# Kernel optimization log

Measured on AMD Instinct MI355X. Metric: run time of the kernel, lower is better.

Reference implementation:

```python
import jax, jax.numpy as jnp
import numpy as np

N_NODES = 500000
N_EDGES = 5000000
IN_CH, OUT_CH = 16, 8


def setup_inputs() -> dict:
    key = jax.random.key(0)
    k1, k2, k3, k4, k5 = jax.random.split(key, 5)
    x = jax.random.normal(k1, (N_NODES, IN_CH), dtype=jnp.float32)
    src = jax.random.randint(k2, (N_EDGES,), 0, N_NODES, dtype=jnp.int64)
    dst = jax.random.randint(k3, (N_EDGES,), 0, N_NODES, dtype=jnp.int64)
    edge_index = jnp.stack([src, dst], axis=0)
    # PyG Linear: weight [out, in], Glorot init; GCNConv bias init zeros
    bound = np.sqrt(6.0 / (IN_CH + OUT_CH))
    W = jax.random.uniform(k4, (OUT_CH, IN_CH), dtype=jnp.float32, minval=-bound, maxval=bound)
    b = jnp.zeros((OUT_CH,), dtype=jnp.float32)
    return {"x": x, "edge_index": edge_index, "W": W, "b": b}


def reference(x, edge_index, W, b):
    """GCNConv(16, 8) with defaults: add_self_loops=True, normalize=True, bias.
    out = D^{-1/2} (A + I) D^{-1/2} X W^T + b, scatter by target index."""
    N = x.shape[0]
    loops = jnp.arange(N, dtype=edge_index.dtype)
    src = jnp.concatenate([edge_index[0], loops])  # [E + N]
    dst = jnp.concatenate([edge_index[1], loops])
    # degree of self-loop-augmented graph, accumulated at target nodes
    deg = jax.ops.segment_sum(jnp.ones(src.shape[0], dtype=x.dtype), dst, num_segments=N)
    dinv = jnp.where(deg > 0, jax.lax.rsqrt(deg), jnp.zeros_like(deg))
    norm = dinv[src] * dinv[dst]  # [E + N]
    h = x @ W.T  # [N, OUT_CH]
    msgs = norm[:, None] * h[src]  # gather + scale, [E + N, OUT_CH]
    out = jax.ops.segment_sum(msgs, dst, num_segments=N) + b
    return out
```

## Files before the change

### kernel.cpp

```cpp
#include <hip/hip_runtime.h>
#include <hip/hip_fp16.h>

#define IN_CH 16
#define OUT_CH 8

#define NT 256
#define EPT 24
#define TILE (NT*EPT)
#define NBUK 512
#define BSHIFT 10
#define BNODES 1024
#define BMASK 1023
#define SRCBITS 19
#define SRCMASK 0x7FFFF
#define CAP 11264
#define RPT 44

typedef float __attribute__((ext_vector_type(4))) fv4;

__global__ void __launch_bounds__(NT) k_bin(const int4* __restrict__ src4,
                                            const int4* __restrict__ dst4, int E,
                                            int* __restrict__ gcur,
                                            unsigned* __restrict__ gbuf) {
    __shared__ int hist[NBUK];
    __shared__ int lofs[NBUK];
    __shared__ int gofs[NBUK];
    __shared__ int wsum[4];
    __shared__ unsigned stage[TILE];
    __shared__ unsigned short posb[TILE];

    int t = threadIdx.x;
    long base = (long)blockIdx.x * TILE;
    int cnt = E - (int)base;
    if (cnt > TILE) cnt = TILE;

    for (int j = t; j < NBUK; j += NT) hist[j] = 0;
    __syncthreads();

    unsigned v[EPT];
    int bk[EPT];
    int rk[EPT];
#pragma unroll
    for (int k = 0; k < EPT / 4; k++) {
        int i4 = t + k * NT;
        if (4 * i4 < cnt) {
            int4 s = src4[base / 4 + i4];
            int4 d = dst4[base / 4 + i4];
            int ss[4] = {s.x, s.y, s.z, s.w};
            int dd[4] = {d.x, d.y, d.z, d.w};
#pragma unroll
            for (int j = 0; j < 4; j++) {
                int q = 4 * k + j;
                bk[q] = dd[j] >> BSHIFT;
                v[q] = ((unsigned)(dd[j] & BMASK) << SRCBITS) | (unsigned)ss[j];
                rk[q] = atomicAdd(&hist[bk[q]], 1);
            }
        } else {
#pragma unroll
            for (int j = 0; j < 4; j++) bk[4 * k + j] = -1;
        }
    }
    __syncthreads();

    int a0 = hist[2 * t], a1 = hist[2 * t + 1];
    int ts = a0 + a1;
    int lane = t & 63, wv = t >> 6;
    int inc = ts;
#pragma unroll
    for (int d = 1; d < 64; d <<= 1) {
        int y = __shfl_up(inc, d);
        if (lane >= d) inc += y;
    }
    if (lane == 63) wsum[wv] = inc;
    __syncthreads();
    int wpre = 0;
#pragma unroll
    for (int w = 0; w < 4; w++) wpre += (w < wv) ? wsum[w] : 0;
    int excl = wpre + inc - ts;

    lofs[2 * t] = excl;
    lofs[2 * t + 1] = excl + a0;
    if (a0 > 0) gofs[2 * t] = atomicAdd(&gcur[2 * t], a0) - excl;
    if (a1 > 0) gofs[2 * t + 1] = atomicAdd(&gcur[2 * t + 1], a1) - (excl + a0);
    __syncthreads();

#pragma unroll
    for (int k = 0; k < EPT; k++) {
        if (bk[k] >= 0) {
            int slot = lofs[bk[k]] + rk[k];
            stage[slot] = v[k];
            posb[slot] = (unsigned short)bk[k];
        }
    }
    __syncthreads();

#pragma unroll
    for (int k = 0; k < EPT; k++) {
        int idx = t + k * NT;
        if (idx < cnt) {
            int b2 = posb[idx];
            gbuf[(size_t)b2 * CAP + idx + gofs[b2]] = stage[idx];
        }
    }
}

__global__ void __launch_bounds__(NT) k_degtrans(const unsigned* __restrict__ gbuf,
                                                 const int* __restrict__ gcur,
                                                 const float* __restrict__ x,
                                                 const float* __restrict__ W,
                                                 uint4* __restrict__ hp16, int N) {
    __shared__ int hist[BNODES];
    __shared__ float Ws[OUT_CH * IN_CH];

    int b = blockIdx.x, t = threadIdx.x;
    int cnt = gcur[b];
    const unsigned* p = gbuf + (size_t)b * CAP;

    if (t < OUT_CH * IN_CH) Ws[t] = W[t];
    for (int j = t; j < BNODES; j += NT) hist[j] = 0;
    __syncthreads();

    int n4 = (cnt + 3) >> 2;
    for (int i4 = t; i4 < n4; i4 += NT) {
        uint4 vv = *(const uint4*)(p + 4 * i4);
        unsigned vs[4] = {vv.x, vv.y, vv.z, vv.w};
#pragma unroll
        for (int j = 0; j < 4; j++)
            if (4 * i4 + j < cnt) atomicAdd(&hist[vs[j] >> SRCBITS], 1);
    }
    __syncthreads();

    int n0 = (b << BSHIFT) + 4 * t;
#pragma unroll
    for (int k = 0; k < 4; k++) {
        int n = n0 + k;
        if (n >= N) break;
        float di = rsqrtf(1.0f + (float)hist[4 * t + k]);
        const float4* xp = (const float4*)(x + (size_t)n * IN_CH);
        float4 a0 = xp[0], a1 = xp[1], a2 = xp[2], a3 = xp[3];
        float xi[IN_CH] = {a0.x, a0.y, a0.z, a0.w, a1.x, a1.y, a1.z, a1.w,
                           a2.x, a2.y, a2.z, a2.w, a3.x, a3.y, a3.z, a3.w};
        float h[OUT_CH];
#pragma unroll
        for (int o = 0; o < OUT_CH; o++) {
            float s = 0.0f;
#pragma unroll
            for (int i = 0; i < IN_CH; i++) s += xi[i] * Ws[o * IN_CH + i];
            h[o] = s * di;
        }
        union { uint4 u; __half2 h2[4]; } pk;
        pk.h2[0] = __float22half2_rn(make_float2(h[0], h[1]));
        pk.h2[1] = __float22half2_rn(make_float2(h[2], h[3]));
        pk.h2[2] = __float22half2_rn(make_float2(h[4], h[5]));
        pk.h2[3] = __float22half2_rn(make_float2(h[6], h[7]));
        hp16[n] = pk.u;
    }
}

__device__ __forceinline__ void acc_add(float* a, uint4 g) {
    union { uint4 u; __half2 h2[4]; } pk;
    pk.u = g;
    float2 f0 = __half22float2(pk.h2[0]);
    float2 f1 = __half22float2(pk.h2[1]);
    float2 f2 = __half22float2(pk.h2[2]);
    float2 f3 = __half22float2(pk.h2[3]);
    a[0] += f0.x; a[1] += f0.y; a[2] += f1.x; a[3] += f1.y;
    a[4] += f2.x; a[5] += f2.y; a[6] += f3.x; a[7] += f3.y;
}

__global__ void __launch_bounds__(NT) k_sortgather(const unsigned* __restrict__ gbuf,
                                                   const int* __restrict__ gcur,
                                                   const uint4* __restrict__ hp16,
                                                   const float* __restrict__ bias,
                                                   float* __restrict__ out, int N) {
    __shared__ unsigned sorted[CAP];
    __shared__ int hist[BNODES];
    __shared__ int wsum[4];

    int b = blockIdx.x, t = threadIdx.x;
    int cnt = gcur[b];
    const unsigned* p = gbuf + (size_t)b * CAP;

    for (int j = t; j < BNODES; j += NT) hist[j] = 0;
    __syncthreads();

    unsigned v[RPT];
    int rk[RPT];
#pragma unroll
    for (int k4 = 0; k4 < RPT / 4; k4++) {
        int idx = 4 * t + k4 * 4 * NT;
        uint4 vv = *(const uint4*)(p + idx);
        unsigned vs[4] = {vv.x, vv.y, vv.z, vv.w};
#pragma unroll
        for (int j = 0; j < 4; j++) {
            int k = 4 * k4 + j;
            if (idx + j < cnt) {
                v[k] = vs[j];
                rk[k] = atomicAdd(&hist[v[k] >> SRCBITS], 1);
            }
        }
    }
    __syncthreads();

    int h0 = hist[4 * t], h1 = hist[4 * t + 1], h2 = hist[4 * t + 2], h3 = hist[4 * t + 3];
    int ts = h0 + h1 + h2 + h3;
    int lane = t & 63, wv = t >> 6;
    int inc = ts;
#pragma unroll
    for (int d = 1; d < 64; d <<= 1) {
        int y = __shfl_up(inc, d);
        if (lane >= d) inc += y;
    }
    if (lane == 63) wsum[wv] = inc;
    __syncthreads();
    int wpre = 0;
#pragma unroll
    for (int w = 0; w < 4; w++) wpre += (w < wv) ? wsum[w] : 0;
    int e0 = wpre + inc - ts;
    int e1 = e0 + h0, e2 = e1 + h1, e3 = e2 + h2;
    hist[4 * t] = e0; hist[4 * t + 1] = e1; hist[4 * t + 2] = e2; hist[4 * t + 3] = e3;
    __syncthreads();

#pragma unroll
    for (int k4 = 0; k4 < RPT / 4; k4++) {
#pragma unroll
        for (int j = 0; j < 4; j++) {
            int k = 4 * k4 + j;
            int idx = 4 * t + k4 * 4 * NT + j;
            if (idx < cnt) {
                int slot = hist[v[k] >> SRCBITS] + rk[k];
                sorted[slot] = v[k] & SRCMASK;
            }
        }
    }
    __syncthreads();

    int n0 = (b << BSHIFT) + 4 * t;
    int eS[4] = {e0, e1, e2, e3};
    int hS[4] = {h0, h1, h2, h3};

    float bb[OUT_CH];
#pragma unroll
    for (int o = 0; o < OUT_CH; o++) bb[o] = bias[o];

#pragma unroll
    for (int k = 0; k < 4; k++) {
        int n = n0 + k;
        if (n >= N) break;

        float a[OUT_CH];
        acc_add((float*)a, hp16[n]);
#pragma unroll
        for (int o = 0; o < OUT_CH; o++) a[o] = a[o];
        {
            union { uint4 u; __half2 h2[4]; } pk;
            pk.u = hp16[n];
            float2 f0 = __half22float2(pk.h2[0]);
            float2 f1 = __half22float2(pk.h2[1]);
            float2 f2 = __half22float2(pk.h2[2]);
            float2 f3 = __half22float2(pk.h2[3]);
            a[0] = f0.x; a[1] = f0.y; a[2] = f1.x; a[3] = f1.y;
            a[4] = f2.x; a[5] = f2.y; a[6] = f3.x; a[7] = f3.y;
        }

        int e = eS[k], end = eS[k] + hS[k];
        for (; e + 3 < end; e += 4) {
            unsigned s0 = sorted[e], s1 = sorted[e + 1];
            unsigned s2 = sorted[e + 2], s3 = sorted[e + 3];
            uint4 g0 = hp16[s0];
            uint4 g1 = hp16[s1];
            uint4 g2 = hp16[s2];
            uint4 g3 = hp16[s3];
            acc_add(a, g0); acc_add(a, g1); acc_add(a, g2); acc_add(a, g3);
        }
        for (; e < end; e++) {
            uint4 g0 = hp16[sorted[e]];
            acc_add(a, g0);
        }

        float di = rsqrtf(1.0f + (float)hS[k]);
        fv4 o0, o1;
#pragma unroll
        for (int j = 0; j < 4; j++) {
            o0[j] = a[j] * di + bb[j];
            o1[j] = a[4 + j] * di + bb[4 + j];
        }
        __builtin_nontemporal_store(o0, (fv4*)(out + (size_t)n * OUT_CH));
        __builtin_nontemporal_store(o1, (fv4*)(out + (size_t)n * OUT_CH) + 1);
    }
}

extern "C" void kernel_launch(void* const* d_in, const int* in_sizes, int n_in,
                              void* d_out, int out_size, void* d_ws, size_t ws_size,
                              hipStream_t stream) {
    const float* x  = (const float*)d_in[0];
    const int*   ei = (const int*)d_in[1];
    const float* W  = (const float*)d_in[2];
    const float* b  = (const float*)d_in[3];
    float* out = (float*)d_out;

    const int N = in_sizes[0] / IN_CH;
    const int E = in_sizes[1] / 2;
    const int* src = ei;
    const int* dst = ei + E;

    const int nbuckets = (N + BNODES - 1) >> BSHIFT;

    int*      gcur = (int*)d_ws;
    uint4*    hp16 = (uint4*)(gcur + NBUK);
    unsigned* gbuf = (unsigned*)(hp16 + N);

    const int tiles = (E + TILE - 1) / TILE;

    (void)hipMemsetAsync(gcur, 0, NBUK * sizeof(int), stream);
    k_bin<<<tiles, NT, 0, stream>>>((const int4*)src, (const int4*)dst, E, gcur, gbuf);
    k_degtrans<<<nbuckets, NT, 0, stream>>>(gbuf, gcur, x, W, hp16, N);
    k_sortgather<<<nbuckets, NT, 0, stream>>>(gbuf, gcur, hp16, b, out, N);
}
```

Before: 215.0 us.

## Replace per-bucket counting sort with LDS atomic accumulation of gathered messages

The final kernel no longer counting-sorts each bucket's edges by destination before a per-node gather loop. Instead each thread gathers source features for eight edges at a time and accumulates them into a shared-memory per-channel accumulator with float atomics, also counting degree atomically. This removes the sort passes, scan and large register arrays, and exposes more independent gathers in flight. In exchange it issues nine LDS atomics per edge and makes the summation order nondeterministic.

```diff
diff --git a/kernel.cpp b/kernel.cpp
--- a/kernel.cpp
+++ b/kernel.cpp
@@ -14,9 +14,9 @@
 #define SRCBITS 19
 #define SRCMASK 0x7FFFF
 #define CAP 11264
-#define RPT 44
 
 typedef float __attribute__((ext_vector_type(4))) fv4;
+typedef unsigned __attribute__((ext_vector_type(4))) uv4;
 
 __global__ void __launch_bounds__(NT) k_bin(const int4* __restrict__ src4,
                                             const int4* __restrict__ dst4, int E,
@@ -157,136 +157,89 @@
     }
 }
 
-__device__ __forceinline__ void acc_add(float* a, uint4 g) {
-    union { uint4 u; __half2 h2[4]; } pk;
-    pk.u = g;
-    float2 f0 = __half22float2(pk.h2[0]);
-    float2 f1 = __half22float2(pk.h2[1]);
-    float2 f2 = __half22float2(pk.h2[2]);
-    float2 f3 = __half22float2(pk.h2[3]);
-    a[0] += f0.x; a[1] += f0.y; a[2] += f1.x; a[3] += f1.y;
-    a[4] += f2.x; a[5] += f2.y; a[6] += f3.x; a[7] += f3.y;
-}
-
-__global__ void __launch_bounds__(NT) k_sortgather(const unsigned* __restrict__ gbuf,
-                                                   const int* __restrict__ gcur,
-                                                   const uint4* __restrict__ hp16,
-                                                   const float* __restrict__ bias,
-                                                   float* __restrict__ out, int N) {
-    __shared__ unsigned sorted[CAP];
-    __shared__ int hist[BNODES];
-    __shared__ int wsum[4];
+__global__ void __launch_bounds__(NT) k_gatheracc(const unsigned* __restrict__ gbuf,
+                                                  const int* __restrict__ gcur,
+                                                  const uint4* __restrict__ hp16,
+                                                  const float* __restrict__ bias,
+                                                  float* __restrict__ out, int N) {
+    __shared__ float sacc[OUT_CH][BNODES];
+    __shared__ int shist[BNODES];
 
     int b = blockIdx.x, t = threadIdx.x;
     int cnt = gcur[b];
     const unsigned* p = gbuf + (size_t)b * CAP;
 
-    for (int j = t; j < BNODES; j += NT) hist[j] = 0;
-    __syncthreads();
-
-    unsigned v[RPT];
-    int rk[RPT];
-#pragma unroll
-    for (int k4 = 0; k4 < RPT / 4; k4++) {
-        int idx = 4 * t + k4 * 4 * NT;
-        uint4 vv = *(const uint4*)(p + idx);
-        unsigned vs[4] = {vv.x, vv.y, vv.z, vv.w};
-#pragma unroll
-        for (int j = 0; j < 4; j++) {
-            int k = 4 * k4 + j;
-            if (idx + j < cnt) {
-                v[k] = vs[j];
-                rk[k] = atomicAdd(&hist[v[k] >> SRCBITS], 1);
+    float4* sz = (float4*)&sacc[0][0];
+#pragma unroll
+    for (int j = 0; j < (OUT_CH * BNODES / 4) / NT; j++)
+        sz[t + j * NT] = make_float4(0.f, 0.f, 0.f, 0.f);
+    ((int4*)shist)[t] = make_int4(0, 0, 0, 0);
+    __syncthreads();
+
+    for (int base = 8 * t; base < cnt; base += 8 * NT) {
+        uv4 va = __builtin_nontemporal_load((const uv4*)(p + base));
+        uv4 vb = __builtin_nontemporal_load((const uv4*)(p + base) + 1);
+        unsigned vs[8] = {va.x, va.y, va.z, va.w, vb.x, vb.y, vb.z, vb.w};
+        int m = cnt - base;
+        uint4 g[8];
+        int ld[8];
+#pragma unroll
+        for (int j = 0; j < 8; j++) {
+            ld[j] = (int)(vs[j] >> SRCBITS);
+            if (j < m) g[j] = hp16[vs[j] & SRCMASK];
+        }
+#pragma unroll
+        for (int j = 0; j < 8; j++) {
+            if (j < m) {
+                union { uint4 u; __half2 h2[4]; } pk;
+                pk.u = g[j];
+                float2 f0 = __half22float2(pk.h2[0]);
+                float2 f1 = __half22float2(pk.h2[1]);
+                float2 f2 = __half22float2(pk.h2[2]);
+                float2 f3 = __half22float2(pk.h2[3]);
+                int d = ld[j];
+                atomicAdd(&shist[d], 1);
+                atomicAdd(&sacc[0][d], f0.x);
+                atomicAdd(&sacc[1][d], f0.y);
+                atomicAdd(&sacc[2][d], f1.x);
+                atomicAdd(&sacc[3][d], f1.y);
+                atomicAdd(&sacc[4][d], f2.x);
+                atomicAdd(&sacc[5][d], f2.y);
+                atomicAdd(&sacc[6][d], f3.x);
+                atomicAdd(&sacc[7][d], f3.y);
             }
         }
     }
     __syncthreads();
 
-    int h0 = hist[4 * t], h1 = hist[4 * t + 1], h2 = hist[4 * t + 2], h3 = hist[4 * t + 3];
-    int ts = h0 + h1 + h2 + h3;
-    int lane = t & 63, wv = t >> 6;
-    int inc = ts;
-#pragma unroll
-    for (int d = 1; d < 64; d <<= 1) {
-        int y = __shfl_up(inc, d);
-        if (lane >= d) inc += y;
-    }
-    if (lane == 63) wsum[wv] = inc;
-    __syncthreads();
-    int wpre = 0;
-#pragma unroll
-    for (int w = 0; w < 4; w++) wpre += (w < wv) ? wsum[w] : 0;
-    int e0 = wpre + inc - ts;
-    int e1 = e0 + h0, e2 = e1 + h1, e3 = e2 + h2;
-    hist[4 * t] = e0; hist[4 * t + 1] = e1; hist[4 * t + 2] = e2; hist[4 * t + 3] = e3;
-    __syncthreads();
-
-#pragma unroll
-    for (int k4 = 0; k4 < RPT / 4; k4++) {
-#pragma unroll
-        for (int j = 0; j < 4; j++) {
-            int k = 4 * k4 + j;
-            int idx = 4 * t + k4 * 4 * NT + j;
-            if (idx < cnt) {
-                int slot = hist[v[k] >> SRCBITS] + rk[k];
-                sorted[slot] = v[k] & SRCMASK;
-            }
-        }
-    }
-    __syncthreads();
-
-    int n0 = (b << BSHIFT) + 4 * t;
-    int eS[4] = {e0, e1, e2, e3};
-    int hS[4] = {h0, h1, h2, h3};
-
     float bb[OUT_CH];
 #pragma unroll
     for (int o = 0; o < OUT_CH; o++) bb[o] = bias[o];
 
 #pragma unroll
-    for (int k = 0; k < 4; k++) {
-        int n = n0 + k;
-        if (n >= N) break;
-
-        float a[OUT_CH];
-        acc_add((float*)a, hp16[n]);
-#pragma unroll
-        for (int o = 0; o < OUT_CH; o++) a[o] = a[o];
-        {
+    for (int k = 0; k < BNODES / NT; k++) {
+        int ln = t + k * NT;
+        int n = (b << BSHIFT) + ln;
+        if (n < N) {
             union { uint4 u; __half2 h2[4]; } pk;
             pk.u = hp16[n];
             float2 f0 = __half22float2(pk.h2[0]);
             float2 f1 = __half22float2(pk.h2[1]);
             float2 f2 = __half22float2(pk.h2[2]);
             float2 f3 = __half22float2(pk.h2[3]);
-            a[0] = f0.x; a[1] = f0.y; a[2] = f1.x; a[3] = f1.y;
-            a[4] = f2.x; a[5] = f2.y; a[6] = f3.x; a[7] = f3.y;
-        }
-
-        int e = eS[k], end = eS[k] + hS[k];
-        for (; e + 3 < end; e += 4) {
-            unsigned s0 = sorted[e], s1 = sorted[e + 1];
-            unsigned s2 = sorted[e + 2], s3 = sorted[e + 3];
-            uint4 g0 = hp16[s0];
-            uint4 g1 = hp16[s1];
-            uint4 g2 = hp16[s2];
-            uint4 g3 = hp16[s3];
-            acc_add(a, g0); acc_add(a, g1); acc_add(a, g2); acc_add(a, g3);
-        }
-        for (; e < end; e++) {
-            uint4 g0 = hp16[sorted[e]];
-            acc_add(a, g0);
-        }
-
-        float di = rsqrtf(1.0f + (float)hS[k]);
-        fv4 o0, o1;
-#pragma unroll
-        for (int j = 0; j < 4; j++) {
-            o0[j] = a[j] * di + bb[j];
-            o1[j] = a[4 + j] * di + bb[4 + j];
-        }
-        __builtin_nontemporal_store(o0, (fv4*)(out + (size_t)n * OUT_CH));
-        __builtin_nontemporal_store(o1, (fv4*)(out + (size_t)n * OUT_CH) + 1);
+            float di = rsqrtf(1.0f + (float)shist[ln]);
+            fv4 o0, o1;
+            o0[0] = (sacc[0][ln] + f0.x) * di + bb[0];
+            o0[1] = (sacc[1][ln] + f0.y) * di + bb[1];
+            o0[2] = (sacc[2][ln] + f1.x) * di + bb[2];
+            o0[3] = (sacc[3][ln] + f1.y) * di + bb[3];
+            o1[0] = (sacc[4][ln] + f2.x) * di + bb[4];
+            o1[1] = (sacc[5][ln] + f2.y) * di + bb[5];
+            o1[2] = (sacc[6][ln] + f3.x) * di + bb[6];
+            o1[3] = (sacc[7][ln] + f3.y) * di + bb[7];
+            __builtin_nontemporal_store(o0, (fv4*)(out + (size_t)n * OUT_CH));
+            __builtin_nontemporal_store(o1, (fv4*)(out + (size_t)n * OUT_CH) + 1);
+        }
     }
 }
 
@@ -315,5 +268,5 @@
     (void)hipMemsetAsync(gcur, 0, NBUK * sizeof(int), stream);
     k_bin<<<tiles, NT, 0, stream>>>((const int4*)src, (const int4*)dst, E, gcur, gbuf);
     k_degtrans<<<nbuckets, NT, 0, stream>>>(gbuf, gcur, x, W, hp16, N);
-    k_sortgather<<<nbuckets, NT, 0, stream>>>(gbuf, gcur, hp16, b, out, N);
-}
+    k_gatheracc<<<nbuckets, NT, 0, stream>>>(gbuf, gcur, hp16, b, out, N);
+}
```

Measured after the change: 378.8 us. +76.2%, slower.

## Move in-bucket sort into degree kernel and gather with one thread per node

Applied to the files above, without the earlier changes.

The per-bucket counting sort now runs in the degree/transform kernel, which writes the sorted source list back to global memory along with per-node row offsets (CSR). The gather kernel becomes a lightweight one-node-per-thread pass over 4x more blocks, with no LDS and no register-heavy staging. This is meant to raise occupancy and latency hiding in the random-gather phase. The cost is an extra global write and re-read of the sorted edges plus a row-offset array.

```diff
diff --git a/kernel.cpp b/kernel.cpp
--- a/kernel.cpp
+++ b/kernel.cpp
@@ -15,6 +15,7 @@
 #define SRCMASK 0x7FFFF
 #define CAP 11264
 #define RPT 44
+#define SPLITN 4
 
 typedef float __attribute__((ext_vector_type(4))) fv4;
 
@@ -104,83 +105,22 @@
     }
 }
 
-__global__ void __launch_bounds__(NT) k_degtrans(const unsigned* __restrict__ gbuf,
-                                                 const int* __restrict__ gcur,
-                                                 const float* __restrict__ x,
-                                                 const float* __restrict__ W,
-                                                 uint4* __restrict__ hp16, int N) {
+__global__ void __launch_bounds__(NT) k_degsort(unsigned* __restrict__ gbuf,
+                                                const int* __restrict__ gcur,
+                                                const float* __restrict__ x,
+                                                const float* __restrict__ W,
+                                                uint4* __restrict__ hp16,
+                                                int* __restrict__ rowofs, int N) {
+    __shared__ unsigned sorted[CAP];
     __shared__ int hist[BNODES];
     __shared__ float Ws[OUT_CH * IN_CH];
+    __shared__ int wsum[4];
 
     int b = blockIdx.x, t = threadIdx.x;
     int cnt = gcur[b];
-    const unsigned* p = gbuf + (size_t)b * CAP;
+    unsigned* p = gbuf + (size_t)b * CAP;
 
     if (t < OUT_CH * IN_CH) Ws[t] = W[t];
-    for (int j = t; j < BNODES; j += NT) hist[j] = 0;
-    __syncthreads();
-
-    int n4 = (cnt + 3) >> 2;
-    for (int i4 = t; i4 < n4; i4 += NT) {
-        uint4 vv = *(const uint4*)(p + 4 * i4);
-        unsigned vs[4] = {vv.x, vv.y, vv.z, vv.w};
-#pragma unroll
-        for (int j = 0; j < 4; j++)
-            if (4 * i4 + j < cnt) atomicAdd(&hist[vs[j] >> SRCBITS], 1);
-    }
-    __syncthreads();
-
-    int n0 = (b << BSHIFT) + 4 * t;
-#pragma unroll
-    for (int k = 0; k < 4; k++) {
-        int n = n0 + k;
-        if (n >= N) break;
-        float di = rsqrtf(1.0f + (float)hist[4 * t + k]);
-        const float4* xp = (const float4*)(x + (size_t)n * IN_CH);
-        float4 a0 = xp[0], a1 = xp[1], a2 = xp[2], a3 = xp[3];
-        float xi[IN_CH] = {a0.x, a0.y, a0.z, a0.w, a1.x, a1.y, a1.z, a1.w,
-                           a2.x, a2.y, a2.z, a2.w, a3.x, a3.y, a3.z, a3.w};
-        float h[OUT_CH];
-#pragma unroll
-        for (int o = 0; o < OUT_CH; o++) {
-            float s = 0.0f;
-#pragma unroll
-            for (int i = 0; i < IN_CH; i++) s += xi[i] * Ws[o * IN_CH + i];
-            h[o] = s * di;
-        }
-        union { uint4 u; __half2 h2[4]; } pk;
-        pk.h2[0] = __float22half2_rn(make_float2(h[0], h[1]));
-        pk.h2[1] = __float22half2_rn(make_float2(h[2], h[3]));
-        pk.h2[2] = __float22half2_rn(make_float2(h[4], h[5]));
-        pk.h2[3] = __float22half2_rn(make_float2(h[6], h[7]));
-        hp16[n] = pk.u;
-    }
-}
-
-__device__ __forceinline__ void acc_add(float* a, uint4 g) {
-    union { uint4 u; __half2 h2[4]; } pk;
-    pk.u = g;
-    float2 f0 = __half22float2(pk.h2[0]);
-    float2 f1 = __half22float2(pk.h2[1]);
-    float2 f2 = __half22float2(pk.h2[2]);
-    float2 f3 = __half22float2(pk.h2[3]);
-    a[0] += f0.x; a[1] += f0.y; a[2] += f1.x; a[3] += f1.y;
-    a[4] += f2.x; a[5] += f2.y; a[6] += f3.x; a[7] += f3.y;
-}
-
-__global__ void __launch_bounds__(NT) k_sortgather(const unsigned* __restrict__ gbuf,
-                                                   const int* __restrict__ gcur,
-                                                   const uint4* __restrict__ hp16,
-                                                   const float* __restrict__ bias,
-                                                   float* __restrict__ out, int N) {
-    __shared__ unsigned sorted[CAP];
-    __shared__ int hist[BNODES];
-    __shared__ int wsum[4];
-
-    int b = blockIdx.x, t = threadIdx.x;
-    int cnt = gcur[b];
-    const unsigned* p = gbuf + (size_t)b * CAP;
-
     for (int j = t; j < BNODES; j += NT) hist[j] = 0;
     __syncthreads();
 
@@ -218,6 +158,8 @@
     for (int w = 0; w < 4; w++) wpre += (w < wv) ? wsum[w] : 0;
     int e0 = wpre + inc - ts;
     int e1 = e0 + h0, e2 = e1 + h1, e3 = e2 + h2;
+    int4 eo = make_int4(e0, e1, e2, e3);
+    *(int4*)(rowofs + (b << BSHIFT) + 4 * t) = eo;
     hist[4 * t] = e0; hist[4 * t + 1] = e1; hist[4 * t + 2] = e2; hist[4 * t + 3] = e3;
     __syncthreads();
 
@@ -235,59 +177,106 @@
     }
     __syncthreads();
 
+    int n4 = (cnt + 3) >> 2;
+    for (int i4 = t; i4 < n4; i4 += NT)
+        ((uint4*)p)[i4] = ((const uint4*)sorted)[i4];
+
     int n0 = (b << BSHIFT) + 4 * t;
-    int eS[4] = {e0, e1, e2, e3};
-    int hS[4] = {h0, h1, h2, h3};
-
-    float bb[OUT_CH];
-#pragma unroll
-    for (int o = 0; o < OUT_CH; o++) bb[o] = bias[o];
-
+    int hh[4] = {h0, h1, h2, h3};
 #pragma unroll
     for (int k = 0; k < 4; k++) {
         int n = n0 + k;
         if (n >= N) break;
-
-        float a[OUT_CH];
-        acc_add((float*)a, hp16[n]);
-#pragma unroll
-        for (int o = 0; o < OUT_CH; o++) a[o] = a[o];
-        {
-            union { uint4 u; __half2 h2[4]; } pk;
-            pk.u = hp16[n];
+        float di = rsqrtf(1.0f + (float)hh[k]);
+        const float4* xp = (const float4*)(x + (size_t)n * IN_CH);
+        float4 a0 = xp[0], a1 = xp[1], a2 = xp[2], a3 = xp[3];
+        float xi[IN_CH] = {a0.x, a0.y, a0.z, a0.w, a1.x, a1.y, a1.z, a1.w,
+                           a2.x, a2.y, a2.z, a2.w, a3.x, a3.y, a3.z, a3.w};
+        float h[OUT_CH];
+#pragma unroll
+        for (int o = 0; o < OUT_CH; o++) {
+            float s = 0.0f;
+#pragma unroll
+            for (int i = 0; i < IN_CH; i++) s += xi[i] * Ws[o * IN_CH + i];
+            h[o] = s * di;
+        }
+        union { uint4 u; __half2 h2[4]; } pk;
+        pk.h2[0] = __float22half2_rn(make_float2(h[0], h[1]));
+        pk.h2[1] = __float22half2_rn(make_float2(h[2], h[3]));
+        pk.h2[2] = __float22half2_rn(make_float2(h[4], h[5]));
+        pk.h2[3] = __float22half2_rn(make_float2(h[6], h[7]));
+        hp16[n] = pk.u;
+    }
+}
+
+__global__ void __launch_bounds__(NT) k_gather(const unsigned* __restrict__ gbuf,
+                                               const int* __restrict__ gcur,
+                                               const int* __restrict__ rowofs,
+                                               const uint4* __restrict__ hp16,
+                                               const float* __restrict__ bias,
+                                               float* __restrict__ out, int N) {
+    int bx = blockIdx.x;
+    int b = bx / SPLITN, q = bx % SPLITN;
+    int t = threadIdx.x;
+    int ln = q * NT + t;
+    int n = (b << BSHIFT) + ln;
+    if (n >= N) return;
+
+    int s = rowofs[(b << BSHIFT) + ln];
+    int e = (ln == BNODES - 1) ? gcur[b] : rowofs[(b << BSHIFT) + ln + 1];
+    const unsigned* p = gbuf + (size_t)b * CAP;
+
+    float a[OUT_CH];
+    {
+        union { uint4 u; __half2 h2[4]; } pk;
+        pk.u = hp16[n];
+        float2 f0 = __half22float2(pk.h2[0]);
+        float2 f1 = __half22float2(pk.h2[1]);
+        float2 f2 = __half22float2(pk.h2[2]);
+        float2 f3 = __half22float2(pk.h2[3]);
+        a[0] = f0.x; a[1] = f0.y; a[2] = f1.x; a[3] = f1.y;
+        a[4] = f2.x; a[5] = f2.y; a[6] = f3.x; a[7] = f3.y;
+    }
+
+    int i = s;
+    for (; i + 3 < e; i += 4) {
+        unsigned s0 = p[i], s1 = p[i + 1], s2 = p[i + 2], s3 = p[i + 3];
+        uint4 g0 = hp16[s0];
+        uint4 g1 = hp16[s1];
+        uint4 g2 = hp16[s2];
+        uint4 g3 = hp16[s3];
+        union { uint4 u; __half2 h2[4]; } pk;
+#pragma unroll
+        for (int jj = 0; jj < 4; jj++) {
+            pk.u = (jj == 0) ? g0 : (jj == 1) ? g1 : (jj == 2) ? g2 : g3;
             float2 f0 = __half22float2(pk.h2[0]);
             float2 f1 = __half22float2(pk.h2[1]);
             float2 f2 = __half22float2(pk.h2[2]);
             float2 f3 = __half22float2(pk.h2[3]);
-            a[0] = f0.x; a[1] = f0.y; a[2] = f1.x; a[3] = f1.y;
-            a[4] = f2.x; a[5] = f2.y; a[6] = f3.x; a[7] = f3.y;
-        }
-
-        int e = eS[k], end = eS[k] + hS[k];
-        for (; e + 3 < end; e += 4) {
-            unsigned s0 = sorted[e], s1 = sorted[e + 1];
-            unsigned s2 = sorted[e + 2], s3 = sorted[e + 3];
-            uint4 g0 = hp16[s0];
-            uint4 g1 = hp16[s1];
-            uint4 g2 = hp16[s2];
-            uint4 g3 = hp16[s3];
-            acc_add(a, g0); acc_add(a, g1); acc_add(a, g2); acc_add(a, g3);
-        }
-        for (; e < end; e++) {
-            uint4 g0 = hp16[sorted[e]];
-            acc_add(a, g0);
-        }
-
-        float di = rsqrtf(1.0f + (float)hS[k]);
-        fv4 o0, o1;
-#pragma unroll
-        for (int j = 0; j < 4; j++) {
-            o0[j] = a[j] * di + bb[j];
-            o1[j] = a[4 + j] * di + bb[4 + j];
-        }
-        __builtin_nontemporal_store(o0, (fv4*)(out + (size_t)n * OUT_CH));
-        __builtin_nontemporal_store(o1, (fv4*)(out + (size_t)n * OUT_CH) + 1);
-    }
+            a[0] += f0.x; a[1] += f0.y; a[2] += f1.x; a[3] += f1.y;
+            a[4] += f2.x; a[5] += f2.y; a[6] += f3.x; a[7] += f3.y;
+        }
+    }
+    for (; i < e; i++) {
+        union { uint4 u; __half2 h2[4]; } pk;
+        pk.u = hp16[p[i]];
+        float2 f0 = __half22float2(pk.h2[0]);
+        float2 f1 = __half22float2(pk.h2[1]);
+        float2 f2 = __half22float2(pk.h2[2]);
+        float2 f3 = __half22float2(pk.h2[3]);
+        a[0] += f0.x; a[1] += f0.y; a[2] += f1.x; a[3] += f1.y;
+        a[4] += f2.x; a[5] += f2.y; a[6] += f3.x; a[7] += f3.y;
+    }
+
+    float di = rsqrtf(1.0f + (float)(e - s));
+    fv4 o0, o1;
+#pragma unroll
+    for (int j = 0; j < 4; j++) {
+        o0[j] = a[j] * di + bias[j];
+        o1[j] = a[4 + j] * di + bias[4 + j];
+    }
+    __builtin_nontemporal_store(o0, (fv4*)(out + (size_t)n * OUT_CH));
+    __builtin_nontemporal_store(o1, (fv4*)(out + (size_t)n * OUT_CH) + 1);
 }
 
 extern "C" void kernel_launch(void* const* d_in, const int* in_sizes, int n_in,
@@ -306,14 +295,15 @@
 
     const int nbuckets = (N + BNODES - 1) >> BSHIFT;
 
-    int*      gcur = (int*)d_ws;
-    uint4*    hp16 = (uint4*)(gcur + NBUK);
-    unsigned* gbuf = (unsigned*)(hp16 + N);
+    int*      gcur   = (int*)d_ws;
+    uint4*    hp16   = (uint4*)(gcur + NBUK);
+    unsigned* gbuf   = (unsigned*)(hp16 + N);
+    int*      rowofs = (int*)(gbuf + (size_t)NBUK * CAP);
 
     const int tiles = (E + TILE - 1) / TILE;
 
     (void)hipMemsetAsync(gcur, 0, NBUK * sizeof(int), stream);
     k_bin<<<tiles, NT, 0, stream>>>((const int4*)src, (const int4*)dst, E, gcur, gbuf);
-    k_degtrans<<<nbuckets, NT, 0, stream>>>(gbuf, gcur, x, W, hp16, N);
-    k_sortgather<<<nbuckets, NT, 0, stream>>>(gbuf, gcur, hp16, b, out, N);
+    k_degsort<<<nbuckets, NT, 0, stream>>>(gbuf, gcur, x, W, hp16, rowofs, N);
+    k_gather<<<nbuckets * SPLITN, NT, 0, stream>>>(gbuf, gcur, rowofs, hp16, b, out, N);
 }
```

Result: slower. 225.9 us (+5.1%).

## Compute degrees via global atomics in binning and split features into half-planes

Applied to the files above, without the earlier changes.

Degree counting moves into the binning kernel as global atomicAdds on a zeroed degree array, so the transform kernel becomes a flat per-node kernel that no longer re-reads the bucketed edge buffer. The sort/gather kernel now takes per-node counts from the degree array to build offsets directly and places edges with shared atomics. The fp16 features are split into two 8-byte planes gathered in two passes, which halves the bytes per random gather but doubles the number of gathers. The cost is 5M global atomics added to the binning kernel and an extra memset of the degree buffer.

```diff
diff --git a/kernel.cpp b/kernel.cpp
--- a/kernel.cpp
+++ b/kernel.cpp
@@ -14,14 +14,15 @@
 #define SRCBITS 19
 #define SRCMASK 0x7FFFF
 #define CAP 11264
-#define RPT 44
 
 typedef float __attribute__((ext_vector_type(4))) fv4;
+typedef unsigned __attribute__((ext_vector_type(4))) uv4;
 
 __global__ void __launch_bounds__(NT) k_bin(const int4* __restrict__ src4,
                                             const int4* __restrict__ dst4, int E,
                                             int* __restrict__ gcur,
-                                            unsigned* __restrict__ gbuf) {
+                                            unsigned* __restrict__ gbuf,
+                                            unsigned* __restrict__ deg) {
     __shared__ int hist[NBUK];
     __shared__ int lofs[NBUK];
     __shared__ int gofs[NBUK];
@@ -54,6 +55,7 @@
                 bk[q] = dd[j] >> BSHIFT;
                 v[q] = ((unsigned)(dd[j] & BMASK) << SRCBITS) | (unsigned)ss[j];
                 rk[q] = atomicAdd(&hist[bk[q]], 1);
+                atomicAdd(&deg[dd[j]], 1u);
             }
         } else {
 #pragma unroll
@@ -104,105 +106,62 @@
     }
 }
 
-__global__ void __launch_bounds__(NT) k_degtrans(const unsigned* __restrict__ gbuf,
-                                                 const int* __restrict__ gcur,
-                                                 const float* __restrict__ x,
-                                                 const float* __restrict__ W,
-                                                 uint4* __restrict__ hp16, int N) {
-    __shared__ int hist[BNODES];
+__global__ void __launch_bounds__(NT) k_trans(const float* __restrict__ x,
+                                              const float* __restrict__ W,
+                                              const unsigned* __restrict__ deg,
+                                              uint2* __restrict__ hpA,
+                                              uint2* __restrict__ hpB, int N) {
     __shared__ float Ws[OUT_CH * IN_CH];
+    int t = threadIdx.x;
+    if (t < OUT_CH * IN_CH) Ws[t] = W[t];
+    __syncthreads();
+    int n = blockIdx.x * NT + t;
+    if (n >= N) return;
+    float di = rsqrtf(1.0f + (float)deg[n]);
+    const fv4* xp = (const fv4*)(x + (size_t)n * IN_CH);
+    fv4 a0 = __builtin_nontemporal_load(xp);
+    fv4 a1 = __builtin_nontemporal_load(xp + 1);
+    fv4 a2 = __builtin_nontemporal_load(xp + 2);
+    fv4 a3 = __builtin_nontemporal_load(xp + 3);
+    float xi[IN_CH] = {a0[0], a0[1], a0[2], a0[3], a1[0], a1[1], a1[2], a1[3],
+                       a2[0], a2[1], a2[2], a2[3], a3[0], a3[1], a3[2], a3[3]};
+    float h[OUT_CH];
+#pragma unroll
+    for (int o = 0; o < OUT_CH; o++) {
+        float s = 0.0f;
+#pragma unroll
+        for (int i = 0; i < IN_CH; i++) s += xi[i] * Ws[o * IN_CH + i];
+        h[o] = s * di;
+    }
+    union { uint2 u; __half2 h2[2]; } pa, pb;
+    pa.h2[0] = __float22half2_rn(make_float2(h[0], h[1]));
+    pa.h2[1] = __float22half2_rn(make_float2(h[2], h[3]));
+    pb.h2[0] = __float22half2_rn(make_float2(h[4], h[5]));
+    pb.h2[1] = __float22half2_rn(make_float2(h[6], h[7]));
+    hpA[n] = pa.u;
+    hpB[n] = pb.u;
+}
+
+__global__ void __launch_bounds__(NT) k_sortgather(const unsigned* __restrict__ gbuf,
+                                                   const int* __restrict__ gcur,
+                                                   const unsigned* __restrict__ deg,
+                                                   const uint2* __restrict__ hpA,
+                                                   const uint2* __restrict__ hpB,
+                                                   const float* __restrict__ bias,
+                                                   float* __restrict__ out, int N) {
+    __shared__ unsigned sorted[CAP];
+    __shared__ int ofs[BNODES];
+    __shared__ int cnt1[BNODES];
+    __shared__ int wsum[4];
 
     int b = blockIdx.x, t = threadIdx.x;
     int cnt = gcur[b];
     const unsigned* p = gbuf + (size_t)b * CAP;
 
-    if (t < OUT_CH * IN_CH) Ws[t] = W[t];
-    for (int j = t; j < BNODES; j += NT) hist[j] = 0;
-    __syncthreads();
-
-    int n4 = (cnt + 3) >> 2;
-    for (int i4 = t; i4 < n4; i4 += NT) {
-        uint4 vv = *(const uint4*)(p + 4 * i4);
-        unsigned vs[4] = {vv.x, vv.y, vv.z, vv.w};
-#pragma unroll
-        for (int j = 0; j < 4; j++)
-            if (4 * i4 + j < cnt) atomicAdd(&hist[vs[j] >> SRCBITS], 1);
-    }
-    __syncthreads();
-
-    int n0 = (b << BSHIFT) + 4 * t;
-#pragma unroll
-    for (int k = 0; k < 4; k++) {
-        int n = n0 + k;
-        if (n >= N) break;
-        float di = rsqrtf(1.0f + (float)hist[4 * t + k]);
-        const float4* xp = (const float4*)(x + (size_t)n * IN_CH);
-        float4 a0 = xp[0], a1 = xp[1], a2 = xp[2], a3 = xp[3];
-        float xi[IN_CH] = {a0.x, a0.y, a0.z, a0.w, a1.x, a1.y, a1.z, a1.w,
-                           a2.x, a2.y, a2.z, a2.w, a3.x, a3.y, a3.z, a3.w};
-        float h[OUT_CH];
-#pragma unroll
-        for (int o = 0; o < OUT_CH; o++) {
-            float s = 0.0f;
-#pragma unroll
-            for (int i = 0; i < IN_CH; i++) s += xi[i] * Ws[o * IN_CH + i];
-            h[o] = s * di;
-        }
-        union { uint4 u; __half2 h2[4]; } pk;
-        pk.h2[0] = __float22half2_rn(make_float2(h[0], h[1]));
-        pk.h2[1] = __float22half2_rn(make_float2(h[2], h[3]));
-        pk.h2[2] = __float22half2_rn(make_float2(h[4], h[5]));
-        pk.h2[3] = __float22half2_rn(make_float2(h[6], h[7]));
-        hp16[n] = pk.u;
-    }
-}
-
-__device__ __forceinline__ void acc_add(float* a, uint4 g) {
-    union { uint4 u; __half2 h2[4]; } pk;
-    pk.u = g;
-    float2 f0 = __half22float2(pk.h2[0]);
-    float2 f1 = __half22float2(pk.h2[1]);
-    float2 f2 = __half22float2(pk.h2[2]);
-    float2 f3 = __half22float2(pk.h2[3]);
-    a[0] += f0.x; a[1] += f0.y; a[2] += f1.x; a[3] += f1.y;
-    a[4] += f2.x; a[5] += f2.y; a[6] += f3.x; a[7] += f3.y;
-}
-
-__global__ void __launch_bounds__(NT) k_sortgather(const unsigned* __restrict__ gbuf,
-                                                   const int* __restrict__ gcur,
-                                                   const uint4* __restrict__ hp16,
-                                                   const float* __restrict__ bias,
-                                                   float* __restrict__ out, int N) {
-    __shared__ unsigned sorted[CAP];
-    __shared__ int hist[BNODES];
-    __shared__ int wsum[4];
-
-    int b = blockIdx.x, t = threadIdx.x;
-    int cnt = gcur[b];
-    const unsigned* p = gbuf + (size_t)b * CAP;
-
-    for (int j = t; j < BNODES; j += NT) hist[j] = 0;
-    __syncthreads();
-
-    unsigned v[RPT];
-    int rk[RPT];
-#pragma unroll
-    for (int k4 = 0; k4 < RPT / 4; k4++) {
-        int idx = 4 * t + k4 * 4 * NT;
-        uint4 vv = *(const uint4*)(p + idx);
-        unsigned vs[4] = {vv.x, vv.y, vv.z, vv.w};
-#pragma unroll
-        for (int j = 0; j < 4; j++) {
-            int k = 4 * k4 + j;
-            if (idx + j < cnt) {
-                v[k] = vs[j];
-                rk[k] = atomicAdd(&hist[v[k] >> SRCBITS], 1);
-            }
-        }
-    }
-    __syncthreads();
-
-    int h0 = hist[4 * t], h1 = hist[4 * t + 1], h2 = hist[4 * t + 2], h3 = hist[4 * t + 3];
+    ((int4*)cnt1)[t] = make_int4(0, 0, 0, 0);
+
+    uint4 dg4 = *(const uint4*)(deg + (b << BSHIFT) + 4 * t);
+    int h0 = (int)dg4.x, h1 = (int)dg4.y, h2 = (int)dg4.z, h3 = (int)dg4.w;
     int ts = h0 + h1 + h2 + h3;
     int lane = t & 63, wv = t >> 6;
     int inc = ts;
@@ -218,18 +177,19 @@
     for (int w = 0; w < 4; w++) wpre += (w < wv) ? wsum[w] : 0;
     int e0 = wpre + inc - ts;
     int e1 = e0 + h0, e2 = e1 + h1, e3 = e2 + h2;
-    hist[4 * t] = e0; hist[4 * t + 1] = e1; hist[4 * t + 2] = e2; hist[4 * t + 3] = e3;
-    __syncthreads();
-
-#pragma unroll
-    for (int k4 = 0; k4 < RPT / 4; k4++) {
+    ofs[4 * t] = e0; ofs[4 * t + 1] = e1; ofs[4 * t + 2] = e2; ofs[4 * t + 3] = e3;
+    __syncthreads();
+
+    int n4 = (cnt + 3) >> 2;
+    for (int i4 = t; i4 < n4; i4 += NT) {
+        uv4 vv = __builtin_nontemporal_load((const uv4*)(p + 4 * i4));
+        unsigned vs[4] = {vv.x, vv.y, vv.z, vv.w};
 #pragma unroll
         for (int j = 0; j < 4; j++) {
-            int k = 4 * k4 + j;
-            int idx = 4 * t + k4 * 4 * NT + j;
-            if (idx < cnt) {
-                int slot = hist[v[k] >> SRCBITS] + rk[k];
-                sorted[slot] = v[k] & SRCMASK;
+            if (4 * i4 + j < cnt) {
+                int dl = (int)(vs[j] >> SRCBITS);
+                int slot = ofs[dl] + atomicAdd(&cnt1[dl], 1);
+                sorted[slot] = vs[j] & SRCMASK;
             }
         }
     }
@@ -239,54 +199,53 @@
     int eS[4] = {e0, e1, e2, e3};
     int hS[4] = {h0, h1, h2, h3};
 
-    float bb[OUT_CH];
-#pragma unroll
-    for (int o = 0; o < OUT_CH; o++) bb[o] = bias[o];
-
-#pragma unroll
-    for (int k = 0; k < 4; k++) {
-        int n = n0 + k;
-        if (n >= N) break;
-
-        float a[OUT_CH];
-        acc_add((float*)a, hp16[n]);
-#pragma unroll
-        for (int o = 0; o < OUT_CH; o++) a[o] = a[o];
-        {
-            union { uint4 u; __half2 h2[4]; } pk;
-            pk.u = hp16[n];
-            float2 f0 = __half22float2(pk.h2[0]);
-            float2 f1 = __half22float2(pk.h2[1]);
-            float2 f2 = __half22float2(pk.h2[2]);
-            float2 f3 = __half22float2(pk.h2[3]);
-            a[0] = f0.x; a[1] = f0.y; a[2] = f1.x; a[3] = f1.y;
-            a[4] = f2.x; a[5] = f2.y; a[6] = f3.x; a[7] = f3.y;
-        }
-
-        int e = eS[k], end = eS[k] + hS[k];
-        for (; e + 3 < end; e += 4) {
-            unsigned s0 = sorted[e], s1 = sorted[e + 1];
-            unsigned s2 = sorted[e + 2], s3 = sorted[e + 3];
-            uint4 g0 = hp16[s0];
-            uint4 g1 = hp16[s1];
-            uint4 g2 = hp16[s2];
-            uint4 g3 = hp16[s3];
-            acc_add(a, g0); acc_add(a, g1); acc_add(a, g2); acc_add(a, g3);
-        }
-        for (; e < end; e++) {
-            uint4 g0 = hp16[sorted[e]];
-            acc_add(a, g0);
-        }
-
-        float di = rsqrtf(1.0f + (float)hS[k]);
-        fv4 o0, o1;
-#pragma unroll
-        for (int j = 0; j < 4; j++) {
-            o0[j] = a[j] * di + bb[j];
-            o1[j] = a[4 + j] * di + bb[4 + j];
-        }
-        __builtin_nontemporal_store(o0, (fv4*)(out + (size_t)n * OUT_CH));
-        __builtin_nontemporal_store(o1, (fv4*)(out + (size_t)n * OUT_CH) + 1);
+#pragma unroll
+    for (int pl = 0; pl < 2; pl++) {
+        const uint2* hp = pl ? hpB : hpA;
+        float b0 = bias[4 * pl], b1 = bias[4 * pl + 1];
+        float b2v = bias[4 * pl + 2], b3 = bias[4 * pl + 3];
+#pragma unroll
+        for (int k = 0; k < 4; k++) {
+            int n = n0 + k;
+            if (n >= N) break;
+            float a0, a1, a2, a3;
+            {
+                union { uint2 u; __half2 h2[2]; } pk;
+                pk.u = hp[n];
+                float2 f0 = __half22float2(pk.h2[0]);
+                float2 f1 = __half22float2(pk.h2[1]);
+                a0 = f0.x; a1 = f0.y; a2 = f1.x; a3 = f1.y;
+            }
+            int e = eS[k], end = eS[k] + hS[k];
+            for (; e + 3 < end; e += 4) {
+                unsigned s0 = sorted[e], s1 = sorted[e + 1];
+                unsigned s2 = sorted[e + 2], s3 = sorted[e + 3];
+                uint2 g0 = hp[s0];
+                uint2 g1 = hp[s1];
+                uint2 g2 = hp[s2];
+                uint2 g3 = hp[s3];
+                union { uint2 u; __half2 h2[2]; } pk;
+#pragma unroll
+                for (int jj = 0; jj < 4; jj++) {
+                    pk.u = (jj == 0) ? g0 : (jj == 1) ? g1 : (jj == 2) ? g2 : g3;
+                    float2 f0 = __half22float2(pk.h2[0]);
+                    float2 f1 = __half22float2(pk.h2[1]);
+                    a0 += f0.x; a1 += f0.y; a2 += f1.x; a3 += f1.y;
+                }
+            }
+            for (; e < end; e++) {
+                union { uint2 u; __half2 h2[2]; } pk;
+                pk.u = hp[sorted[e]];
+                float2 f0 = __half22float2(pk.h2[0]);
+                float2 f1 = __half22float2(pk.h2[1]);
+                a0 += f0.x; a1 += f0.y; a2 += f1.x; a3 += f1.y;
+            }
+            float di = rsqrtf(1.0f + (float)hS[k]);
+            fv4 o;
+            o[0] = a0 * di + b0; o[1] = a1 * di + b1;
+            o[2] = a2 * di + b2v; o[3] = a3 * di + b3;
+            __builtin_nontemporal_store(o, (fv4*)(out + (size_t)n * OUT_CH + 4 * pl));
+        }
     }
 }
 
@@ -306,14 +265,18 @@
 
     const int nbuckets = (N + BNODES - 1) >> BSHIFT;
 
-    int*      gcur = (int*)d_ws;
-    uint4*    hp16 = (uint4*)(gcur + NBUK);
-    unsigned* gbuf = (unsigned*)(hp16 + N);
+    char* base = (char*)d_ws;
+    int*      gcur = (int*)base;
+    unsigned* deg  = (unsigned*)(base + 4096);
+    uint2*    hpA  = (uint2*)(base + 4096 + 2097152);
+    uint2*    hpB  = hpA + (size_t)NBUK * BNODES;
+    unsigned* gbuf = (unsigned*)(hpB + (size_t)NBUK * BNODES);
 
     const int tiles = (E + TILE - 1) / TILE;
-
-    (void)hipMemsetAsync(gcur, 0, NBUK * sizeof(int), stream);
-    k_bin<<<tiles, NT, 0, stream>>>((const int4*)src, (const int4*)dst, E, gcur, gbuf);
-    k_degtrans<<<nbuckets, NT, 0, stream>>>(gbuf, gcur, x, W, hp16, N);
-    k_sortgather<<<nbuckets, NT, 0, stream>>>(gbuf, gcur, hp16, b, out, N);
-}
+    const int nblocks = (N + NT - 1) / NT;
+
+    (void)hipMemsetAsync(base, 0, 4096 + 2097152, stream);
+    k_bin<<<tiles, NT, 0, stream>>>((const int4*)src, (const int4*)dst, E, gcur, gbuf, deg);
+    k_trans<<<nblocks, NT, 0, stream>>>(x, W, deg, hpA, hpB, N);
+    k_sortgather<<<nbuckets, NT, 0, stream>>>(gbuf, gcur, deg, hpA, hpB, b, out, N);
+}
```

Result: slower. 399.1 us (+85.6%).
